# Optimization experiments

Measured on AMD Instinct MI355X. Metric: run time of the kernel, lower is better.

The kernel has to match this reference:

```python
import jax, jax.numpy as jnp
import numpy as np
import math

# Model dims (from init_kwargs + mamba_ssm Mamba2 defaults)
D_MODEL = 1024
EXPAND = 2
HEADDIM = 64
D_STATE = 64
D_CONV = 4
NGROUPS = 1
D_INNER = EXPAND * D_MODEL            # 2048
NHEADS = D_INNER // HEADDIM           # 32
CONV_DIM = D_INNER + 2 * NGROUPS * D_STATE   # 2176
D_IN_PROJ = 2 * D_INNER + 2 * NGROUPS * D_STATE + NHEADS  # 4256
BATCH, SEQLEN = 4, 2048
RMS_EPS = 1.1920929e-07   # torch.finfo(float32).eps (nn.RMSNorm eps=None)
GNORM_EPS = 1e-5          # mamba_ssm RMSNormGated eps


def _rmsnorm(x, w, eps):
    return x * jax.lax.rsqrt(jnp.mean(x * x, axis=-1, keepdims=True) + eps) * w


def setup_inputs() -> dict:
    key = jax.random.key(0)
    ks = jax.random.split(key, 8)
    x = jax.random.normal(ks[0], (BATCH, SEQLEN, D_MODEL), jnp.float32)
    # router MLP (Linear(d_model,32) -> SiLU -> Linear(32,3))
    r_w1 = jax.random.normal(ks[1], (32, D_MODEL), jnp.float32) / math.sqrt(D_MODEL)
    r_b1 = jnp.zeros((32,), jnp.float32)
    r_w2 = jax.random.normal(ks[2], (3, 32), jnp.float32) / math.sqrt(32)
    r_b2 = jnp.zeros((3,), jnp.float32)
    # Mamba2 params
    in_proj_w = jax.random.normal(ks[3], (D_IN_PROJ, D_MODEL), jnp.float32) / math.sqrt(D_MODEL)
    conv_w = jax.random.normal(ks[4], (CONV_DIM, D_CONV), jnp.float32) * 0.2
    conv_b = jnp.zeros((CONV_DIM,), jnp.float32)
    dt_bias = jax.random.normal(ks[5], (NHEADS,), jnp.float32) * 0.1
    # OrthoSSM multi-scale override: A_log[i] = log(0.001 * 2**i)
    A_log = jnp.log(0.001 * (2.0 ** jnp.arange(NHEADS, dtype=jnp.float32)))
    D_param = jnp.ones((NHEADS,), jnp.float32)
    gnorm_w = jnp.ones((D_INNER,), jnp.float32)
    out_proj_w = jax.random.normal(ks[6], (D_MODEL, D_INNER), jnp.float32) / math.sqrt(D_INNER)
    norm_w = jnp.ones((D_MODEL,), jnp.float32)
    return {"x": x, "norm_w": norm_w, "r_w1": r_w1, "r_b1": r_b1, "r_w2": r_w2,
            "r_b2": r_b2, "in_proj_w": in_proj_w, "conv_w": conv_w, "conv_b": conv_b,
            "dt_bias": dt_bias, "A_log": A_log, "D_param": D_param,
            "gnorm_w": gnorm_w, "out_proj_w": out_proj_w}


def _forward(x, norm_w, r_w1, r_b1, r_w2, r_b2, in_proj_w, conv_w, conv_b,
             dt_bias, A_log, D_param, gnorm_w, out_proj_w):
    B, S, Dm = x.shape
    x_norm = _rmsnorm(x, norm_w, RMS_EPS)
    # --- router: mean-pool -> tiny MLP -> softmax over 3 tiers ---
    h = jax.nn.silu(x_norm.mean(axis=1) @ r_w1.T + r_b1)
    probs = jax.nn.softmax(h @ r_w2.T + r_b2, axis=-1)   # [B,3]
    p_fast = probs[:, 0][:, None, None]
    p_mamba = (probs[:, 1] + probs[:, 2])[:, None, None]
    # --- Mamba2(x_norm) ---
    zxbcdt = x_norm @ in_proj_w.T                         # [B,S,4256]
    z, xBC, dt = jnp.split(zxbcdt, [D_INNER, D_INNER + CONV_DIM], axis=-1)
    # causal depthwise conv1d (kernel 4) + SiLU
    conv = jax.lax.conv_general_dilated(
        xBC.transpose(0, 2, 1), conv_w[:, None, :], (1,), [(D_CONV - 1, 0)],
        feature_group_count=CONV_DIM)                      # [B,CONV_DIM,S]
    xBC = jax.nn.silu(conv.transpose(0, 2, 1) + conv_b)    # [B,S,CONV_DIM]
    xh, Bmat, Cmat = jnp.split(xBC, [D_INNER, D_INNER + NGROUPS * D_STATE], axis=-1)
    xh = xh.reshape(B, S, NHEADS, HEADDIM)                 # [B,S,H,P]
    dt = jax.nn.softplus(dt + dt_bias)                     # [B,S,H]
    A = -jnp.exp(A_log)                                    # [H]
    dA = jnp.exp(dt * A)                                   # [B,S,H]

    def step(hstate, inp):
        dA_t, dt_t, x_t, B_t, C_t = inp
        # hstate: [B,H,P,N]
        hstate = hstate * dA_t[..., None, None] \
                 + (dt_t[..., None] * x_t)[..., None] * B_t[:, None, None, :]
        y_t = jnp.einsum('bhpn,bn->bhp', hstate, C_t)
        return hstate, y_t

    h0 = jnp.zeros((B, NHEADS, HEADDIM, D_STATE), x.dtype)
    xs = (dA.transpose(1, 0, 2), dt.transpose(1, 0, 2), xh.transpose(1, 0, 2, 3),
          Bmat.transpose(1, 0, 2), Cmat.transpose(1, 0, 2))
    _, ys = jax.lax.scan(step, h0, xs)                     # [S,B,H,P]
    y = ys.transpose(1, 0, 2, 3) + D_param[:, None] * xh   # D skip connection
    y = y.reshape(B, S, D_INNER)
    # gated RMSNorm: norm(y * silu(z)) * weight
    yg = y * jax.nn.silu(z)
    yg = _rmsnorm(yg, gnorm_w, GNORM_EPS)
    mamba_out = yg @ out_proj_w.T                          # [B,S,D]
    out = p_fast * x_norm + p_mamba * mamba_out
    return x + out


def reference(x, norm_w, r_w1, r_b1, r_w2, r_b2, in_proj_w, conv_w, conv_b,
              dt_bias, A_log, D_param, gnorm_w, out_proj_w):
    return _forward(x, norm_w, r_w1, r_b1, r_w2, r_b2, in_proj_w, conv_w, conv_b,
                    dt_bias, A_log, D_param, gnorm_w, out_proj_w)
```

## Files before the change

kernel.cpp:

```cpp
#include <hip/hip_runtime.h>
#include <math.h>

typedef __bf16 bf16;
typedef __bf16 bf16x8 __attribute__((ext_vector_type(8)));
typedef __bf16 bf16x4 __attribute__((ext_vector_type(4)));
typedef float f32x4 __attribute__((ext_vector_type(4)));

#define DEV static __device__ __forceinline__
#define AS1 __attribute__((address_space(1)))
#define AS3 __attribute__((address_space(3)))

constexpr int kBatch = 4, kSeq = 2048, kDModel = 1024;
constexpr int kDInner = 2048, kHeads = 32;
constexpr int kConvDim = 2176, kDInProj = 4256, kNPad1 = 4352;
constexpr int kRows = kBatch * kSeq;
constexpr int kChunk = 64, kNChunk = kSeq / kChunk;
constexpr float kRmsEps = 1.1920929e-07f;
constexpr float kGnEps = 1e-5f;

DEV float siluf(float x) { return x / (1.f + expf(-x)); }

DEV float block_reduce_sum(float v, float* red, int tid) {
#pragma unroll
  for (int m = 1; m < 64; m <<= 1) v += __shfl_xor(v, m);
  if ((tid & 63) == 0) red[tid >> 6] = v;
  __syncthreads();
  return red[0] + red[1] + red[2] + red[3];
}

__global__ __launch_bounds__(256) void k_rmsnorm(const float* __restrict__ x,
                                                 const float* __restrict__ nw,
                                                 bf16* __restrict__ xnb,
                                                 float* __restrict__ rs) {
  const int row = blockIdx.x;
  const int tid = threadIdx.x;
  float4 v = ((const float4*)(x + (size_t)row * kDModel))[tid];
  __shared__ float red[4];
  float ss = block_reduce_sum(v.x * v.x + v.y * v.y + v.z * v.z + v.w * v.w, red, tid);
  float scale = rsqrtf(ss * (1.f / kDModel) + kRmsEps);
  if (tid == 0) rs[row] = scale;
  float4 wv = ((const float4*)nw)[tid];
  bf16x4 ov;
  ov[0] = (bf16)(v.x * scale * wv.x);
  ov[1] = (bf16)(v.y * scale * wv.y);
  ov[2] = (bf16)(v.z * scale * wv.z);
  ov[3] = (bf16)(v.w * scale * wv.w);
  *(bf16x4*)(xnb + (size_t)row * kDModel + tid * 4) = ov;
}

__global__ __launch_bounds__(128) void k_pool1(const bf16* __restrict__ xnb,
                                               float* __restrict__ part) {
  const int g = blockIdx.x, b = blockIdx.y;
  const int tid = threadIdx.x;
  const bf16* base = xnb + ((size_t)b * kSeq + (size_t)g * 32) * kDModel + tid * 8;
  float acc[8] = {0, 0, 0, 0, 0, 0, 0, 0};
  for (int r = 0; r < 32; ++r) {
    bf16x8 v = *(const bf16x8*)(base + (size_t)r * kDModel);
#pragma unroll
    for (int j = 0; j < 8; ++j) acc[j] += (float)v[j];
  }
  float* o = part + ((size_t)b * 64 + g) * kDModel + tid * 8;
#pragma unroll
  for (int j = 0; j < 8; ++j) o[j] = acc[j];
}

__global__ __launch_bounds__(256) void k_pool2(const float* __restrict__ part,
                                               float* __restrict__ mean) {
  const int idx = blockIdx.x * 256 + threadIdx.x;
  const int b = idx >> 10, d = idx & 1023;
  float s = 0.f;
  for (int g = 0; g < 64; ++g) s += part[((size_t)b * 64 + g) * kDModel + d];
  mean[idx] = s * (1.f / kSeq);
}

__global__ __launch_bounds__(128) void k_router(const float* __restrict__ mean,
                                                const float* __restrict__ w1,
                                                const float* __restrict__ b1,
                                                const float* __restrict__ w2,
                                                const float* __restrict__ b2,
                                                float* __restrict__ pfm) {
  __shared__ float hbuf[4][32];
  __shared__ float logit[4][3];
  const int t = threadIdx.x;
  {
    int b = t >> 5, j = t & 31;
    float s = b1[j];
    for (int d = 0; d < kDModel; ++d) s += mean[b * kDModel + d] * w1[j * kDModel + d];
    hbuf[b][j] = siluf(s);
  }
  __syncthreads();
  if (t < 12) {
    int b = t / 3, k = t % 3;
    float s = b2[k];
    for (int j = 0; j < 32; ++j) s += hbuf[b][j] * w2[k * 32 + j];
    logit[b][k] = s;
  }
  __syncthreads();
  if (t < 4) {
    float m = fmaxf(logit[t][0], fmaxf(logit[t][1], logit[t][2]));
    float e0 = expf(logit[t][0] - m), e1 = expf(logit[t][1] - m), e2 = expf(logit[t][2] - m);
    float inv = 1.f / (e0 + e1 + e2);
    pfm[t] = e0 * inv;
    pfm[4 + t] = (e1 + e2) * inv;
  }
}

__global__ __launch_bounds__(256) void k_castpad_w1(const float* __restrict__ w,
                                                    bf16* __restrict__ wb) {
  const size_t idx = (size_t)blockIdx.x * 256 + threadIdx.x;
  const int row = (int)(idx >> 10);
  wb[idx] = (bf16)(row < kDInProj ? w[idx] : 0.f);
}

__global__ __launch_bounds__(256) void k_cast_w2(const float* __restrict__ w,
                                                 const float* __restrict__ gw,
                                                 bf16* __restrict__ wb) {
  const size_t i4 = (size_t)blockIdx.x * 256 + threadIdx.x;
  const int k4 = (int)((i4 * 4) & (kDInner - 1));
  float4 v = ((const float4*)w)[i4];
  float4 g = *(const float4*)(gw + k4);
  bf16x4 o;
  o[0] = (bf16)(v.x * g.x); o[1] = (bf16)(v.y * g.y);
  o[2] = (bf16)(v.z * g.z); o[3] = (bf16)(v.w * g.w);
  ((bf16x4*)wb)[i4] = o;
}

template <int WM, int WN, int NF, bool FUSE>
__global__ __launch_bounds__(WM * WN * 64, 4) void k_gemm(
    const bf16* __restrict__ A, const bf16* __restrict__ B,
    bf16* __restrict__ Cb, const float* __restrict__ xres,
    const float* __restrict__ rs, const float* __restrict__ nw,
    const float* __restrict__ pfm, float* __restrict__ outf,
    int K, int Nreal, int ldc, int ntn) {
  constexpr int THREADS = WM * WN * 64;
  constexpr int BM = WM * 64;
  constexpr int BN = WN * NF * 16;
  constexpr int NA = (BM * 4) / THREADS;
  constexpr int NB = (BN * 4) / THREADS;
  constexpr int VMN = NA + NB;
  constexpr int ASZ = (BM / 2) * 64;
  constexpr int BSZ = (BN / 2) * 64;
  __shared__ __align__(16) bf16 lds[3 * ASZ + 3 * BSZ];
  __shared__ float rs2s[BM];
  const int tid = threadIdx.x;
  const int lane = tid & 63, wid = tid >> 6;
  const int wr = wid / WN, wc = wid % WN;
  const int lr = lane & 15, kb = lane >> 4;
  const int cpx = (int)gridDim.x >> 3;
  const int bid = ((int)blockIdx.x & 7) * cpx + ((int)blockIdx.x >> 3);
  const long n0 = (long)(bid % ntn) * BN;
  const long m0 = (long)(bid / ntn) * BM;

  f32x4 acc[4][NF];
#pragma unroll
  for (int i = 0; i < 4; ++i)
#pragma unroll
    for (int j = 0; j < NF; ++j) acc[i][j] = (f32x4){0.f, 0.f, 0.f, 0.f};
  float ssq[4] = {0.f, 0.f, 0.f, 0.f};

  const int nkt = K >> 5;

#define STAGE(pp, kt)                                                          \
  {                                                                            \
    const long koff = (long)(kt)*32;                                           \
    _Pragma("unroll") for (int j = 0; j < NA; ++j) {                           \
      int idx = j * THREADS + tid;                                             \
      int line = idx >> 3, sp = (idx & 7) ^ (line & 7);                        \
      int row = line * 2 + (sp >> 2), ch = sp & 3;                             \
      __builtin_amdgcn_global_load_lds(                                        \
          (const AS1 void*)(A + (m0 + row) * K + koff + ch * 8),               \
          (AS3 void*)((char*)(lds + (pp)*ASZ) + idx * 16), 16, 0, 0);          \
    }                                                                          \
    _Pragma("unroll") for (int j = 0; j < NB; ++j) {                           \
      int idx = j * THREADS + tid;                                             \
      int line = idx >> 3, sp = (idx & 7) ^ (line & 7);                        \
      int row = line * 2 + (sp >> 2), ch = sp & 3;                             \
      __builtin_amdgcn_global_load_lds(                                        \
          (const AS1 void*)(B + (n0 + row) * K + koff + ch * 8),               \
          (AS3 void*)((char*)(lds + 3 * ASZ + (pp)*BSZ) + idx * 16), 16, 0, 0);\
    }                                                                          \
  }
#define LOFF(r) (((r) >> 1) * 128 + (((((r)&1) << 2) | kb) ^ (((r) >> 1) & 7)) * 16)
#define RDA(pp, r) (*(const bf16x8*)((const char*)(lds + (pp)*ASZ) + LOFF(r)))
#define RDB(pp, r) (*(const bf16x8*)((const char*)(lds + 3 * ASZ + (pp)*BSZ) + LOFF(r)))

  STAGE(0, 0);
  STAGE(1, 1);

  int cur = 0;
  for (int t = 0; t < nkt; ++t) {
    if (t + 2 < nkt) {
      int sb = cur + 2; if (sb >= 3) sb -= 3;
      STAGE(sb, t + 2);
      if constexpr (VMN == 3) asm volatile("s_waitcnt vmcnt(6)" ::: "memory");
      else if constexpr (VMN == 4) asm volatile("s_waitcnt vmcnt(8)" ::: "memory");
      else asm volatile("s_waitcnt vmcnt(12)" ::: "memory");
    } else if (t + 1 < nkt) {
      if constexpr (VMN == 3) asm volatile("s_waitcnt vmcnt(3)" ::: "memory");
      else if constexpr (VMN == 4) asm volatile("s_waitcnt vmcnt(4)" ::: "memory");
      else asm volatile("s_waitcnt vmcnt(6)" ::: "memory");
    } else {
      asm volatile("s_waitcnt vmcnt(0)" ::: "memory");
    }
    __builtin_amdgcn_s_barrier();

    bf16x8 af[4], bv[NF];
#pragma unroll
    for (int mf = 0; mf < 4; ++mf) af[mf] = RDA(cur, wr * 64 + mf * 16 + lr);
#pragma unroll
    for (int nf = 0; nf < NF; ++nf) bv[nf] = RDB(cur, wc * 64 + nf * 16 + lr);
    asm volatile("s_waitcnt lgkmcnt(0)" ::: "memory");
    __builtin_amdgcn_sched_barrier(0);
    __builtin_amdgcn_s_barrier();

    if constexpr (FUSE) {
      if (wc == 0) {
#pragma unroll
        for (int mf = 0; mf < 4; ++mf)
#pragma unroll
          for (int e = 0; e < 8; ++e) {
            float f = (float)af[mf][e];
            ssq[mf] = fmaf(f, f, ssq[mf]);
          }
      }
    }
    __builtin_amdgcn_s_setprio(1);
#pragma unroll
    for (int mf = 0; mf < 4; ++mf)
#pragma unroll
      for (int nf = 0; nf < NF; ++nf)
        acc[mf][nf] = __builtin_amdgcn_mfma_f32_16x16x32_bf16(af[mf], bv[nf],
                                                              acc[mf][nf], 0, 0, 0);
    __builtin_amdgcn_s_setprio(0);
    cur = cur + 1 == 3 ? 0 : cur + 1;
  }
#undef STAGE
#undef LOFF
#undef RDA
#undef RDB

  const int rr = kb * 4;
  if constexpr (FUSE) {
    if (wc == 0) {
#pragma unroll
      for (int mf = 0; mf < 4; ++mf) {
        float v = ssq[mf];
        v += __shfl_xor(v, 16);
        v += __shfl_xor(v, 32);
        if (kb == 0) rs2s[wr * 64 + mf * 16 + lr] = rsqrtf(v * (1.f / kDInner) + kGnEps);
      }
    }
    __syncthreads();
    const int bx = (int)(m0 >> 11);
    const float pf = pfm[bx], pm = pfm[4 + bx];
#pragma unroll
    for (int mf = 0; mf < 4; ++mf) {
      long rbase = m0 + wr * 64 + mf * 16 + rr;
      float rsv[4], r2v[4];
#pragma unroll
      for (int j = 0; j < 4; ++j) {
        rsv[j] = rs[rbase + j];
        r2v[j] = rs2s[wr * 64 + mf * 16 + rr + j];
      }
#pragma unroll
      for (int nf = 0; nf < NF; ++nf) {
        int col = (int)n0 + wc * 64 + nf * 16 + lr;
        float wv = nw[col];
#pragma unroll
        for (int j = 0; j < 4; ++j) {
          size_t oi = (size_t)(rbase + j) * kDModel + col;
          float xv = xres[oi];
          outf[oi] = xv + pf * xv * rsv[j] * wv + pm * r2v[j] * acc[mf][nf][j];
        }
      }
    }
  } else {
    __syncthreads();
    bf16* scr = lds + wid * (16 * 72);
    const int srow = lane >> 2, cg = lane & 3;
#pragma unroll
    for (int mf = 0; mf < 4; ++mf) {
#pragma unroll
      for (int nf = 0; nf < NF; ++nf)
#pragma unroll
        for (int j = 0; j < 4; ++j)
          scr[(rr + j) * 72 + nf * 16 + lr] = (bf16)acc[mf][nf][j];
      asm volatile("s_waitcnt lgkmcnt(0)" ::: "memory");
      __builtin_amdgcn_sched_barrier(0);
      int col = (int)n0 + wc * (NF * 16) + cg * 16;
      if (col < Nreal) {
        long grow = m0 + wr * 64 + mf * 16 + srow;
        bf16x8 v0 = *(const bf16x8*)(scr + srow * 72 + cg * 16);
        bf16x8 v1 = *(const bf16x8*)(scr + srow * 72 + cg * 16 + 8);
        *(bf16x8*)(Cb + grow * (long)ldc + col) = v0;
        *(bf16x8*)(Cb + grow * (long)ldc + col + 8) = v1;
      }
      __builtin_amdgcn_sched_barrier(0);
    }
  }
}

__global__ __launch_bounds__(256) void k_convdt(const bf16* __restrict__ zx,
                                                const float* __restrict__ cw,
                                                const float* __restrict__ cb,
                                                bf16* __restrict__ xbc,
                                                const float* __restrict__ dt_bias,
                                                const float* __restrict__ A_log,
                                                float* __restrict__ dt,
                                                float* __restrict__ ldA) {
  const int gid = blockIdx.x * 256 + threadIdx.x;
  if (gid < kRows * 272) {
    const int row = gid / 272;
    const int cg = gid - row * 272;
    const int c0 = cg * 8;
    const int s = row & (kSeq - 1);
    const bf16* base = zx + (size_t)row * kDInProj + kDInner + c0;
    bf16x8 z8 = {};
    bf16x8 r3 = *(const bf16x8*)(base);
    bf16x8 r2 = (s >= 1) ? *(const bf16x8*)(base - kDInProj) : z8;
    bf16x8 r1 = (s >= 2) ? *(const bf16x8*)(base - 2 * kDInProj) : z8;
    bf16x8 r0 = (s >= 3) ? *(const bf16x8*)(base - 3 * kDInProj) : z8;
    bf16x8 o;
#pragma unroll
    for (int e = 0; e < 8; ++e) {
      float4 w = ((const float4*)cw)[c0 + e];
      float a = cb[c0 + e] + w.x * (float)r0[e] + w.y * (float)r1[e] +
                w.z * (float)r2[e] + w.w * (float)r3[e];
      o[e] = (bf16)siluf(a);
    }
    *(bf16x8*)(xbc + (size_t)row * kConvDim + c0) = o;
  } else {
    const int g2 = gid - kRows * 272;
    const int row = g2 >> 2, grp = g2 & 3;
    bf16x8 r8 = *(const bf16x8*)(zx + (size_t)row * kDInProj + (kDInner + kConvDim) + grp * 8);
#pragma unroll
    for (int e = 0; e < 8; ++e) {
      int hh = grp * 8 + e;
      float raw = (float)r8[e] + dt_bias[hh];
      float dtv = (raw > 20.f) ? raw : log1pf(expf(raw));
      dt[row * kHeads + hh] = dtv;
      ldA[row * kHeads + hh] = dtv * -expf(A_log[hh]);
    }
  }
}

__global__ __launch_bounds__(256) void k_chunkA(
    const bf16* __restrict__ xbc, const float* __restrict__ dtb,
    const float* __restrict__ ldab, float* __restrict__ cumbuf,
    float* __restrict__ Tc, bf16* __restrict__ yb, bf16* __restrict__ Sbuf) {
  const int c = blockIdx.x, h = blockIdx.y, b = blockIdx.z;
  const int tid = threadIdx.x;
  const int w = tid >> 6, lane = tid & 63, lr = lane & 15, kb = lane >> 4;
  const int rr = kb * 4;
  const int t0 = c * kChunk;
  __shared__ bf16 Bl[64 * 72], Cl[64 * 72], XT[64 * 72], WBT[64 * 72], Ml[64 * 72];
  __shared__ float cum_s[64], dt_s[64], w_s[64];

  {
    int s = tid >> 2, q = tid & 3;
    const bf16* rowp = xbc + ((size_t)b * kSeq + t0 + s) * kConvDim;
    bf16x8 x0 = *(const bf16x8*)(rowp + h * 64 + q * 16);
    bf16x8 x1 = *(const bf16x8*)(rowp + h * 64 + q * 16 + 8);
    bf16x8 b0 = *(const bf16x8*)(rowp + kDInner + q * 16);
    bf16x8 b1 = *(const bf16x8*)(rowp + kDInner + q * 16 + 8);
    bf16x8 c0 = *(const bf16x8*)(rowp + kDInner + 64 + q * 16);
    bf16x8 c1 = *(const bf16x8*)(rowp + kDInner + 64 + q * 16 + 8);
    *(bf16x8*)(Bl + s * 72 + q * 16) = b0;
    *(bf16x8*)(Bl + s * 72 + q * 16 + 8) = b1;
    *(bf16x8*)(Cl + s * 72 + q * 16) = c0;
    *(bf16x8*)(Cl + s * 72 + q * 16 + 8) = c1;
#pragma unroll
    for (int e = 0; e < 8; ++e) XT[(q * 16 + e) * 72 + s] = x0[e];
#pragma unroll
    for (int e = 0; e < 8; ++e) XT[(q * 16 + 8 + e) * 72 + s] = x1[e];
  }
  if (tid < 64) {
    size_t di = ((size_t)b * kSeq + t0 + tid) * kHeads + h;
    float v = ldab[di];
    float dtv = dtb[di];
#pragma unroll
    for (int o = 1; o < 64; o <<= 1) {
      float u = __shfl_up(v, o);
      if (lane >= o) v += u;
    }
    cum_s[tid] = v;
    dt_s[tid] = dtv;
    float tot = __shfl(v, 63);
    w_s[tid] = expf(tot - v) * dtv;
    cumbuf[(((size_t)b * kHeads + h) * kNChunk + c) * 64 + tid] = v;
    if (tid == 63) Tc[(b * kHeads + h) * kNChunk + c] = expf(v);
  }
  __syncthreads();

#pragma unroll
  for (int i = 0; i < 16; ++i) {
    int e = i * 256 + tid;
    int n = e >> 6, s = e & 63;
    WBT[n * 72 + s] = (bf16)((float)Bl[s * 72 + n] * w_s[s]);
  }

  f32x4 g[4];
#pragma unroll
  for (int nt = 0; nt < 4; ++nt) g[nt] = (f32x4){0.f, 0.f, 0.f, 0.f};
#pragma unroll
  for (int kk = 0; kk < 2; ++kk) {
    bf16x8 a = *(const bf16x8*)(Cl + (w * 16 + lr) * 72 + kk * 32 + kb * 8);
#pragma unroll
    for (int nt = 0; nt < 4; ++nt) {
      bf16x8 bb = *(const bf16x8*)(Bl + (nt * 16 + lr) * 72 + kk * 32 + kb * 8);
      g[nt] = __builtin_amdgcn_mfma_f32_16x16x32_bf16(a, bb, g[nt], 0, 0, 0);
    }
  }
#pragma unroll
  for (int nt = 0; nt < 4; ++nt)
#pragma unroll
    for (int j = 0; j < 4; ++j) {
      int tt = w * 16 + rr + j, ss = nt * 16 + lr;
      float m = (ss <= tt) ? g[nt][j] * expf(cum_s[tt] - cum_s[ss]) * dt_s[ss] : 0.f;
      Ml[tt * 72 + ss] = (bf16)m;
    }
  __syncthreads();

  f32x4 y4[4];
#pragma unroll
  for (int pt = 0; pt < 4; ++pt) y4[pt] = (f32x4){0.f, 0.f, 0.f, 0.f};
#pragma unroll
  for (int kk = 0; kk < 2; ++kk) {
    bf16x8 a = *(const bf16x8*)(Ml + (w * 16 + lr) * 72 + kk * 32 + kb * 8);
#pragma unroll
    for (int pt = 0; pt < 4; ++pt) {
      bf16x8 bb = *(const bf16x8*)(XT + (pt * 16 + lr) * 72 + kk * 32 + kb * 8);
      y4[pt] = __builtin_amdgcn_mfma_f32_16x16x32_bf16(a, bb, y4[pt], 0, 0, 0);
    }
  }
  f32x4 s4[4];
#pragma unroll
  for (int nt = 0; nt < 4; ++nt) s4[nt] = (f32x4){0.f, 0.f, 0.f, 0.f};
#pragma unroll
  for (int kk = 0; kk < 2; ++kk) {
    bf16x8 a = *(const bf16x8*)(XT + (w * 16 + lr) * 72 + kk * 32 + kb * 8);
#pragma unroll
    for (int nt = 0; nt < 4; ++nt) {
      bf16x8 bb = *(const bf16x8*)(WBT + (nt * 16 + lr) * 72 + kk * 32 + kb * 8);
      s4[nt] = __builtin_amdgcn_mfma_f32_16x16x32_bf16(a, bb, s4[nt], 0, 0, 0);
    }
  }
#pragma unroll
  for (int pt = 0; pt < 4; ++pt)
#pragma unroll
    for (int j = 0; j < 4; ++j) {
      Bl[(w * 16 + rr + j) * 72 + pt * 16 + lr] = (bf16)y4[pt][j];
      Cl[(w * 16 + rr + j) * 72 + pt * 16 + lr] = (bf16)s4[pt][j];
    }
  __syncthreads();
  {
    int row = tid >> 2, cg = tid & 3;
    bf16x8 v0 = *(const bf16x8*)(Bl + row * 72 + cg * 16);
    bf16x8 v1 = *(const bf16x8*)(Bl + row * 72 + cg * 16 + 8);
    bf16* dst = yb + ((size_t)b * kSeq + t0 + row) * kDInner + h * 64 + cg * 16;
    *(bf16x8*)dst = v0;
    *(bf16x8*)(dst + 8) = v1;
    const size_t sbase = (((size_t)b * kHeads + h) * kNChunk + c) * 4096;
    bf16x8 u0 = *(const bf16x8*)(Cl + row * 72 + cg * 16);
    bf16x8 u1 = *(const bf16x8*)(Cl + row * 72 + cg * 16 + 8);
    bf16* sdst = Sbuf + sbase + row * 64 + cg * 16;
    *(bf16x8*)sdst = u0;
    *(bf16x8*)(sdst + 8) = u1;
  }
}

__global__ __launch_bounds__(256) void k_chunkB(bf16* __restrict__ S,
                                                const float* __restrict__ Tc) {
  const int gid = blockIdx.x * 256 + threadIdx.x;
  const int bh = gid >> 10;
  const int pn = (gid & 1023) << 2;
  bf16* base = S + (size_t)bh * kNChunk * 4096 + pn;
  const float* tc = Tc + bh * kNChunk;
  float4 hh = {0.f, 0.f, 0.f, 0.f};
  bf16x4 s = *(const bf16x4*)(base);
  for (int c = 0; c < kNChunk; ++c) {
    bf16x4 sn = {};
    if (c + 1 < kNChunk) sn = *(const bf16x4*)(base + (size_t)(c + 1) * 4096);
    float t = tc[c];
    bf16x4 ho;
    ho[0] = (bf16)hh.x; ho[1] = (bf16)hh.y; ho[2] = (bf16)hh.z; ho[3] = (bf16)hh.w;
    *(bf16x4*)(base + (size_t)c * 4096) = ho;
    hh.x = t * hh.x + (float)s[0];
    hh.y = t * hh.y + (float)s[1];
    hh.z = t * hh.z + (float)s[2];
    hh.w = t * hh.w + (float)s[3];
    s = sn;
  }
}

__global__ __launch_bounds__(256) void k_chunkC(
    const bf16* __restrict__ xbc, const bf16* __restrict__ zx,
    const float* __restrict__ cumbuf, const bf16* __restrict__ hs,
    const float* __restrict__ Dp, bf16* __restrict__ yb) {
  const int c = blockIdx.x, h = blockIdx.y, b = blockIdx.z;
  const int tid = threadIdx.x;
  const int w = tid >> 6, lane = tid & 63, lr = lane & 15, kb = lane >> 4;
  const int rr = kb * 4;
  const int t0 = c * kChunk;
  __shared__ bf16 Cl[64 * 72];
  __shared__ float ecum[64];
  __shared__ float scrf[64 * 68];
  {
    int s = tid >> 2, q = tid & 3;
    const bf16* rowp = xbc + ((size_t)b * kSeq + t0 + s) * kConvDim + kDInner + 64 + q * 16;
    *(bf16x8*)(Cl + s * 72 + q * 16) = *(const bf16x8*)rowp;
    *(bf16x8*)(Cl + s * 72 + q * 16 + 8) = *(const bf16x8*)(rowp + 8);
  }
  if (tid < 64)
    ecum[tid] = expf(cumbuf[(((size_t)b * kHeads + h) * kNChunk + c) * 64 + tid]);
  __syncthreads();

  const bf16* hbase = hs + (((size_t)b * kHeads + h) * kNChunk + c) * 4096;
  f32x4 acc[4];
#pragma unroll
  for (int pt = 0; pt < 4; ++pt) acc[pt] = (f32x4){0.f, 0.f, 0.f, 0.f};
#pragma unroll
  for (int kk = 0; kk < 2; ++kk) {
    bf16x8 a = *(const bf16x8*)(Cl + (w * 16 + lr) * 72 + kk * 32 + kb * 8);
#pragma unroll
    for (int pt = 0; pt < 4; ++pt) {
      bf16x8 bb = *(const bf16x8*)(hbase + (pt * 16 + lr) * 64 + kk * 32 + kb * 8);
      acc[pt] = __builtin_amdgcn_mfma_f32_16x16x32_bf16(a, bb, acc[pt], 0, 0, 0);
    }
  }
#pragma unroll
  for (int pt = 0; pt < 4; ++pt)
#pragma unroll
    for (int j = 0; j < 4; ++j) {
      int tt = w * 16 + rr + j;
      scrf[tt * 68 + pt * 16 + lr] = ecum[tt] * acc[pt][j];
    }
  __syncthreads();
  {
    const float Dh = Dp[h];
    int row = tid >> 2, cg = tid & 3;
    size_t ri = (size_t)b * kSeq + t0 + row;
    const float* sp = scrf + row * 68 + cg * 16;
    bf16* yp = yb + ri * kDInner + h * 64 + cg * 16;
    const bf16* xp = xbc + ri * kConvDim + h * 64 + cg * 16;
    const bf16* zp = zx + ri * kDInProj + h * 64 + cg * 16;
#pragma unroll
    for (int half = 0; half < 2; ++half) {
      bf16x8 yv = *(const bf16x8*)(yp + half * 8);
      bf16x8 xv = *(const bf16x8*)(xp + half * 8);
      bf16x8 zv = *(const bf16x8*)(zp + half * 8);
      bf16x8 o;
#pragma unroll
      for (int e = 0; e < 8; ++e) {
        float yfull = (float)yv[e] + sp[half * 8 + e] + Dh * (float)xv[e];
        o[e] = (bf16)(yfull * siluf((float)zv[e]));
      }
      *(bf16x8*)(yp + half * 8) = o;
    }
  }
}

extern "C" void kernel_launch(void* const* d_in, const int* in_sizes, int n_in,
                              void* d_out, int out_size, void* d_ws, size_t ws_size,
                              hipStream_t stream) {
  const float* x = (const float*)d_in[0];
  const float* norm_w = (const float*)d_in[1];
  const float* r_w1 = (const float*)d_in[2];
  const float* r_b1 = (const float*)d_in[3];
  const float* r_w2 = (const float*)d_in[4];
  const float* r_b2 = (const float*)d_in[5];
  const float* in_proj_w = (const float*)d_in[6];
  const float* conv_w = (const float*)d_in[7];
  const float* conv_b = (const float*)d_in[8];
  const float* dt_bias = (const float*)d_in[9];
  const float* A_log = (const float*)d_in[10];
  const float* D_param = (const float*)d_in[11];
  const float* gnorm_w = (const float*)d_in[12];
  const float* out_proj_w = (const float*)d_in[13];
  float* out = (float*)d_out;
  char* ws = (char*)d_ws;

  bf16* xnb     = (bf16*)(ws + 0);
  bf16* w1b     = (bf16*)(ws + 16777216);
  bf16* zx      = (bf16*)(ws + 25690112);
  bf16* xbc     = (bf16*)(ws + 95420416);
  float* dtb    = (float*)(ws + 131072000);
  float* ldab   = (float*)(ws + 132120576);
  float* cumbuf = (float*)(ws + 133169152);
  float* Tcb    = (float*)(ws + 134217728);
  bf16* yb      = (bf16*)(ws + 134234112);
  bf16* Sbuf    = (bf16*)(ws + 167788544);
  bf16* w2b     = (bf16*)(ws + 201342976);
  float* part   = (float*)(ws + 205537280);
  float* meanb  = (float*)(ws + 206585856);
  float* pfm    = (float*)(ws + 206602240);
  float* rsb    = (float*)(ws + 206602368);

  k_rmsnorm<<<kRows, 256, 0, stream>>>(x, norm_w, xnb, rsb);
  k_pool1<<<dim3(64, 4), 128, 0, stream>>>(xnb, part);
  k_pool2<<<16, 256, 0, stream>>>(part, meanb);
  k_router<<<1, 128, 0, stream>>>(meanb, r_w1, r_b1, r_w2, r_b2, pfm);
  k_castpad_w1<<<kNPad1 * kDModel / 256, 256, 0, stream>>>(in_proj_w, w1b);
  k_cast_w2<<<kDModel * kDInner / 1024, 256, 0, stream>>>(out_proj_w, gnorm_w, w2b);
  k_gemm<2, 4, 4, false><<<(kRows / 128) * (kNPad1 / 256), 512, 0, stream>>>(
      xnb, w1b, zx, nullptr, nullptr, nullptr, nullptr, nullptr,
      kDModel, kDInProj, kDInProj, kNPad1 / 256);
  k_convdt<<<(kRows * 272 + kRows * 4) / 256, 256, 0, stream>>>(
      zx, conv_w, conv_b, xbc, dt_bias, A_log, dtb, ldab);
  k_chunkA<<<dim3(kNChunk, kHeads, kBatch), 256, 0, stream>>>(
      xbc, dtb, ldab, cumbuf, Tcb, yb, Sbuf);
  k_chunkB<<<512, 256, 0, stream>>>(Sbuf, Tcb);
  k_chunkC<<<dim3(kNChunk, kHeads, kBatch), 256, 0, stream>>>(
      xbc, zx, cumbuf, Sbuf, D_param, yb);
  k_gemm<1, 2, 4, true><<<(kRows / 64) * (kDModel / 128), 128, 0, stream>>>(
      yb, w2b, nullptr, x, rsb, norm_w, pfm, out,
      kDInner, kDModel, kDModel, kDModel / 128);
}
```

Baseline: 348.8 us.

## Merge prep kernels, interleave LDS reads with MFMA, retile out-proj GEMM

Folds the RMSNorm kernel and both weight-cast kernels into one launch dispatched by block index, removing two launches and their serialisation. The GEMM inner loop now issues the A-fragment LDS reads in stages, with partial lgkmcnt waits, so MFMAs on earlier fragments can overlap the later reads. The out-projection GEMM moves from 1x2 waves with 4 N-fragments to 1x4 waves with 2 N-fragments, giving 256 threads per block for the same tile shape. The GEMM is split into two wrappers with statically sized LDS, which adds code complexity and carries hand-tuned waitcnt assumptions that could be fragile.

Result: no change. 344.6 us (-1.2%).

```diff
diff --git a/kernel.cpp b/kernel.cpp
--- a/kernel.cpp
+++ b/kernel.cpp
@@ -17,6 +17,8 @@
 constexpr int kChunk = 64, kNChunk = kSeq / kChunk;
 constexpr float kRmsEps = 1.1920929e-07f;
 constexpr float kGnEps = 1e-5f;
+constexpr int kW1Blocks = kNPad1 * kDModel / 256;
+constexpr int kW2Blocks = kDModel * kDInner / 1024;
 
 DEV float siluf(float x) { return x / (1.f + expf(-x)); }
 
@@ -28,24 +30,42 @@
   return red[0] + red[1] + red[2] + red[3];
 }
 
-__global__ __launch_bounds__(256) void k_rmsnorm(const float* __restrict__ x,
-                                                 const float* __restrict__ nw,
-                                                 bf16* __restrict__ xnb,
-                                                 float* __restrict__ rs) {
-  const int row = blockIdx.x;
+__global__ __launch_bounds__(256) void k_pre(
+    const float* __restrict__ x, const float* __restrict__ nw,
+    bf16* __restrict__ xnb, float* __restrict__ rs,
+    const float* __restrict__ w1, bf16* __restrict__ w1b,
+    const float* __restrict__ w2, const float* __restrict__ gw,
+    bf16* __restrict__ w2b) {
+  const int blk = blockIdx.x;
   const int tid = threadIdx.x;
-  float4 v = ((const float4*)(x + (size_t)row * kDModel))[tid];
-  __shared__ float red[4];
-  float ss = block_reduce_sum(v.x * v.x + v.y * v.y + v.z * v.z + v.w * v.w, red, tid);
-  float scale = rsqrtf(ss * (1.f / kDModel) + kRmsEps);
-  if (tid == 0) rs[row] = scale;
-  float4 wv = ((const float4*)nw)[tid];
-  bf16x4 ov;
-  ov[0] = (bf16)(v.x * scale * wv.x);
-  ov[1] = (bf16)(v.y * scale * wv.y);
-  ov[2] = (bf16)(v.z * scale * wv.z);
-  ov[3] = (bf16)(v.w * scale * wv.w);
-  *(bf16x4*)(xnb + (size_t)row * kDModel + tid * 4) = ov;
+  if (blk < kRows) {
+    const int row = blk;
+    float4 v = ((const float4*)(x + (size_t)row * kDModel))[tid];
+    __shared__ float red[4];
+    float ss = block_reduce_sum(v.x * v.x + v.y * v.y + v.z * v.z + v.w * v.w, red, tid);
+    float scale = rsqrtf(ss * (1.f / kDModel) + kRmsEps);
+    if (tid == 0) rs[row] = scale;
+    float4 wv = ((const float4*)nw)[tid];
+    bf16x4 ov;
+    ov[0] = (bf16)(v.x * scale * wv.x);
+    ov[1] = (bf16)(v.y * scale * wv.y);
+    ov[2] = (bf16)(v.z * scale * wv.z);
+    ov[3] = (bf16)(v.w * scale * wv.w);
+    *(bf16x4*)(xnb + (size_t)row * kDModel + tid * 4) = ov;
+  } else if (blk < kRows + kW1Blocks) {
+    const size_t idx = (size_t)(blk - kRows) * 256 + tid;
+    const int row = (int)(idx >> 10);
+    w1b[idx] = (bf16)(row < kDInProj ? w1[idx] : 0.f);
+  } else {
+    const size_t i4 = (size_t)(blk - kRows - kW1Blocks) * 256 + tid;
+    const int k4 = (int)((i4 * 4) & (kDInner - 1));
+    float4 v = ((const float4*)w2)[i4];
+    float4 g = *(const float4*)(gw + k4);
+    bf16x4 o;
+    o[0] = (bf16)(v.x * g.x); o[1] = (bf16)(v.y * g.y);
+    o[2] = (bf16)(v.z * g.z); o[3] = (bf16)(v.w * g.w);
+    ((bf16x4*)w2b)[i4] = o;
+  }
 }
 
 __global__ __launch_bounds__(128) void k_pool1(const bf16* __restrict__ xnb,
@@ -105,33 +125,13 @@
   }
 }
 
-__global__ __launch_bounds__(256) void k_castpad_w1(const float* __restrict__ w,
-                                                    bf16* __restrict__ wb) {
-  const size_t idx = (size_t)blockIdx.x * 256 + threadIdx.x;
-  const int row = (int)(idx >> 10);
-  wb[idx] = (bf16)(row < kDInProj ? w[idx] : 0.f);
-}
-
-__global__ __launch_bounds__(256) void k_cast_w2(const float* __restrict__ w,
-                                                 const float* __restrict__ gw,
-                                                 bf16* __restrict__ wb) {
-  const size_t i4 = (size_t)blockIdx.x * 256 + threadIdx.x;
-  const int k4 = (int)((i4 * 4) & (kDInner - 1));
-  float4 v = ((const float4*)w)[i4];
-  float4 g = *(const float4*)(gw + k4);
-  bf16x4 o;
-  o[0] = (bf16)(v.x * g.x); o[1] = (bf16)(v.y * g.y);
-  o[2] = (bf16)(v.z * g.z); o[3] = (bf16)(v.w * g.w);
-  ((bf16x4*)wb)[i4] = o;
-}
-
 template <int WM, int WN, int NF, bool FUSE>
-__global__ __launch_bounds__(WM * WN * 64, 4) void k_gemm(
-    const bf16* __restrict__ A, const bf16* __restrict__ B,
-    bf16* __restrict__ Cb, const float* __restrict__ xres,
-    const float* __restrict__ rs, const float* __restrict__ nw,
-    const float* __restrict__ pfm, float* __restrict__ outf,
-    int K, int Nreal, int ldc, int ntn) {
+DEV void gemm_body(bf16* lds, float* rs2s,
+                   const bf16* __restrict__ A, const bf16* __restrict__ B,
+                   bf16* __restrict__ Cb, const float* __restrict__ xres,
+                   const float* __restrict__ rs, const float* __restrict__ nw,
+                   const float* __restrict__ pfm, float* __restrict__ outf,
+                   int K, int Nreal, int ldc, int ntn) {
   constexpr int THREADS = WM * WN * 64;
   constexpr int BM = WM * 64;
   constexpr int BN = WN * NF * 16;
@@ -140,8 +140,6 @@
   constexpr int VMN = NA + NB;
   constexpr int ASZ = (BM / 2) * 64;
   constexpr int BSZ = (BN / 2) * 64;
-  __shared__ __align__(16) bf16 lds[3 * ASZ + 3 * BSZ];
-  __shared__ float rs2s[BM];
   const int tid = threadIdx.x;
   const int lane = tid & 63, wid = tid >> 6;
   const int wr = wid / WN, wc = wid % WN;
@@ -193,45 +191,60 @@
       int sb = cur + 2; if (sb >= 3) sb -= 3;
       STAGE(sb, t + 2);
       if constexpr (VMN == 3) asm volatile("s_waitcnt vmcnt(6)" ::: "memory");
-      else if constexpr (VMN == 4) asm volatile("s_waitcnt vmcnt(8)" ::: "memory");
-      else asm volatile("s_waitcnt vmcnt(12)" ::: "memory");
+      else asm volatile("s_waitcnt vmcnt(8)" ::: "memory");
     } else if (t + 1 < nkt) {
       if constexpr (VMN == 3) asm volatile("s_waitcnt vmcnt(3)" ::: "memory");
-      else if constexpr (VMN == 4) asm volatile("s_waitcnt vmcnt(4)" ::: "memory");
-      else asm volatile("s_waitcnt vmcnt(6)" ::: "memory");
+      else asm volatile("s_waitcnt vmcnt(4)" ::: "memory");
     } else {
       asm volatile("s_waitcnt vmcnt(0)" ::: "memory");
     }
     __builtin_amdgcn_s_barrier();
 
-    bf16x8 af[4], bv[NF];
-#pragma unroll
-    for (int mf = 0; mf < 4; ++mf) af[mf] = RDA(cur, wr * 64 + mf * 16 + lr);
-#pragma unroll
-    for (int nf = 0; nf < NF; ++nf) bv[nf] = RDB(cur, wc * 64 + nf * 16 + lr);
+    bf16x8 bv[NF], af0, af1, af2, af3;
+#pragma unroll
+    for (int nf = 0; nf < NF; ++nf) bv[nf] = RDB(cur, wc * (NF * 16) + nf * 16 + lr);
+    af0 = RDA(cur, wr * 64 + lr);
+    __builtin_amdgcn_sched_barrier(0);
+    af1 = RDA(cur, wr * 64 + 16 + lr);
+    __builtin_amdgcn_sched_barrier(0);
+    asm volatile("s_waitcnt lgkmcnt(1)" ::: "memory");
+    __builtin_amdgcn_sched_barrier(0);
+    __builtin_amdgcn_s_setprio(1);
+#pragma unroll
+    for (int nf = 0; nf < NF; ++nf)
+      acc[0][nf] = __builtin_amdgcn_mfma_f32_16x16x32_bf16(af0, bv[nf], acc[0][nf], 0, 0, 0);
+    af2 = RDA(cur, wr * 64 + 32 + lr);
+    af3 = RDA(cur, wr * 64 + 48 + lr);
+    __builtin_amdgcn_sched_barrier(0);
+    asm volatile("s_waitcnt lgkmcnt(2)" ::: "memory");
+    __builtin_amdgcn_sched_barrier(0);
+#pragma unroll
+    for (int nf = 0; nf < NF; ++nf)
+      acc[1][nf] = __builtin_amdgcn_mfma_f32_16x16x32_bf16(af1, bv[nf], acc[1][nf], 0, 0, 0);
     asm volatile("s_waitcnt lgkmcnt(0)" ::: "memory");
     __builtin_amdgcn_sched_barrier(0);
     __builtin_amdgcn_s_barrier();
+#pragma unroll
+    for (int nf = 0; nf < NF; ++nf)
+      acc[2][nf] = __builtin_amdgcn_mfma_f32_16x16x32_bf16(af2, bv[nf], acc[2][nf], 0, 0, 0);
+#pragma unroll
+    for (int nf = 0; nf < NF; ++nf)
+      acc[3][nf] = __builtin_amdgcn_mfma_f32_16x16x32_bf16(af3, bv[nf], acc[3][nf], 0, 0, 0);
+    __builtin_amdgcn_s_setprio(0);
 
     if constexpr (FUSE) {
       if (wc == 0) {
 #pragma unroll
-        for (int mf = 0; mf < 4; ++mf)
-#pragma unroll
-          for (int e = 0; e < 8; ++e) {
-            float f = (float)af[mf][e];
-            ssq[mf] = fmaf(f, f, ssq[mf]);
-          }
+        for (int e = 0; e < 8; ++e) {
+          float f0 = (float)af0[e], f1 = (float)af1[e];
+          float f2 = (float)af2[e], f3 = (float)af3[e];
+          ssq[0] = fmaf(f0, f0, ssq[0]);
+          ssq[1] = fmaf(f1, f1, ssq[1]);
+          ssq[2] = fmaf(f2, f2, ssq[2]);
+          ssq[3] = fmaf(f3, f3, ssq[3]);
+        }
       }
     }
-    __builtin_amdgcn_s_setprio(1);
-#pragma unroll
-    for (int mf = 0; mf < 4; ++mf)
-#pragma unroll
-      for (int nf = 0; nf < NF; ++nf)
-        acc[mf][nf] = __builtin_amdgcn_mfma_f32_16x16x32_bf16(af[mf], bv[nf],
-                                                              acc[mf][nf], 0, 0, 0);
-    __builtin_amdgcn_s_setprio(0);
     cur = cur + 1 == 3 ? 0 : cur + 1;
   }
 #undef STAGE
@@ -264,7 +277,7 @@
       }
 #pragma unroll
       for (int nf = 0; nf < NF; ++nf) {
-        int col = (int)n0 + wc * 64 + nf * 16 + lr;
+        int col = (int)n0 + wc * (NF * 16) + nf * 16 + lr;
         float wv = nw[col];
 #pragma unroll
         for (int j = 0; j < 4; ++j) {
@@ -298,6 +311,28 @@
       __builtin_amdgcn_sched_barrier(0);
     }
   }
+}
+
+__global__ __launch_bounds__(512, 4) void k_gemm_in(
+    const bf16* __restrict__ A, const bf16* __restrict__ B,
+    bf16* __restrict__ Cb, int K, int Nreal, int ldc, int ntn) {
+  constexpr int ASZ = (128 / 2) * 64, BSZ = (256 / 2) * 64;
+  __shared__ __align__(16) bf16 lds[3 * ASZ + 3 * BSZ];
+  __shared__ float rs2s[128];
+  gemm_body<2, 4, 4, false>(lds, rs2s, A, B, Cb, nullptr, nullptr, nullptr,
+                            nullptr, nullptr, K, Nreal, ldc, ntn);
+}
+
+__global__ __launch_bounds__(256, 4) void k_gemm_out(
+    const bf16* __restrict__ A, const bf16* __restrict__ B,
+    const float* __restrict__ xres, const float* __restrict__ rs,
+    const float* __restrict__ nw, const float* __restrict__ pfm,
+    float* __restrict__ outf, int K, int Nreal, int ldc, int ntn) {
+  constexpr int ASZ = (64 / 2) * 64, BSZ = (128 / 2) * 64;
+  __shared__ __align__(16) bf16 lds[3 * ASZ + 3 * BSZ];
+  __shared__ float rs2s[64];
+  gemm_body<1, 4, 2, true>(lds, rs2s, A, B, nullptr, xres, rs, nw, pfm, outf,
+                           K, Nreal, ldc, ntn);
 }
 
 __global__ __launch_bounds__(256) void k_convdt(const bf16* __restrict__ zx,
@@ -596,15 +631,13 @@
   float* pfm    = (float*)(ws + 206602240);
   float* rsb    = (float*)(ws + 206602368);
 
-  k_rmsnorm<<<kRows, 256, 0, stream>>>(x, norm_w, xnb, rsb);
+  k_pre<<<kRows + kW1Blocks + kW2Blocks, 256, 0, stream>>>(
+      x, norm_w, xnb, rsb, in_proj_w, w1b, out_proj_w, gnorm_w, w2b);
   k_pool1<<<dim3(64, 4), 128, 0, stream>>>(xnb, part);
   k_pool2<<<16, 256, 0, stream>>>(part, meanb);
   k_router<<<1, 128, 0, stream>>>(meanb, r_w1, r_b1, r_w2, r_b2, pfm);
-  k_castpad_w1<<<kNPad1 * kDModel / 256, 256, 0, stream>>>(in_proj_w, w1b);
-  k_cast_w2<<<kDModel * kDInner / 1024, 256, 0, stream>>>(out_proj_w, gnorm_w, w2b);
-  k_gemm<2, 4, 4, false><<<(kRows / 128) * (kNPad1 / 256), 512, 0, stream>>>(
-      xnb, w1b, zx, nullptr, nullptr, nullptr, nullptr, nullptr,
-      kDModel, kDInProj, kDInProj, kNPad1 / 256);
+  k_gemm_in<<<(kRows / 128) * (kNPad1 / 256), 512, 0, stream>>>(
+      xnb, w1b, zx, kDModel, kDInProj, kDInProj, kNPad1 / 256);
   k_convdt<<<(kRows * 272 + kRows * 4) / 256, 256, 0, stream>>>(
       zx, conv_w, conv_b, xbc, dt_bias, A_log, dtb, ldab);
   k_chunkA<<<dim3(kNChunk, kHeads, kBatch), 256, 0, stream>>>(
@@ -612,7 +645,7 @@
   k_chunkB<<<512, 256, 0, stream>>>(Sbuf, Tcb);
   k_chunkC<<<dim3(kNChunk, kHeads, kBatch), 256, 0, stream>>>(
       xbc, zx, cumbuf, Sbuf, D_param, yb);
-  k_gemm<1, 2, 4, true><<<(kRows / 64) * (kDModel / 128), 128, 0, stream>>>(
-      yb, w2b, nullptr, x, rsb, norm_w, pfm, out,
+  k_gemm_out<<<(kRows / 64) * (kDModel / 128), 256, 0, stream>>>(
+      yb, w2b, x, rsb, norm_w, pfm, out,
       kDInner, kDModel, kDModel, kDModel / 128);
 }
```
